# Kernel tuning notes

Measured on AMD Instinct MI355X. Metric: run time of the kernel, lower is better.

Reference implementation:

```python
import jax, jax.numpy as jnp
import numpy as np

N_IMG = 1024
N_VIEWS = 90


def _bilinear(img, yi, xi):
    """Bilinear sample img at float coords (yi=row, xi=col); 0 outside (skimage warp cval=0)."""
    n = img.shape[0]
    y0 = jnp.floor(yi)
    x0 = jnp.floor(xi)
    wy = yi - y0
    wx = xi - x0
    y0i = y0.astype(jnp.int32)
    x0i = x0.astype(jnp.int32)

    def get(yy, xx):
        valid = (yy >= 0) & (yy < n) & (xx >= 0) & (xx < n)
        v = img[jnp.clip(yy, 0, n - 1), jnp.clip(xx, 0, n - 1)]
        return jnp.where(valid, v, jnp.zeros((), img.dtype))

    v00 = get(y0i, x0i)
    v01 = get(y0i, x0i + 1)
    v10 = get(y0i + 1, x0i)
    v11 = get(y0i + 1, x0i + 1)
    return (v00 * (1 - wy) * (1 - wx) + v01 * (1 - wy) * wx
            + v10 * wy * (1 - wx) + v11 * wy * wx)


def radon_jax(image, theta_deg):
    """skimage.transform.radon(image, theta, circle=True) equivalent.
    Rotate image by each angle (bilinear, about center = N//2, inverse map as in
    skimage warp) and sum over rows. Returns sinogram [N, n_angles]."""
    n = image.shape[0]
    center = n // 2
    ang = jnp.deg2rad(theta_deg.astype(image.dtype))
    cos_a = jnp.cos(ang)  # [A]
    sin_a = jnp.sin(ang)
    coords = jnp.arange(n, dtype=image.dtype)
    X, Y = jnp.meshgrid(coords, coords)  # X = col (x), Y = row (y), [N, N]

    def rotate_and_sum(ca, sa):
        # inverse map: src = R @ dst (homogeneous, (x, y) order) as in skimage radon
        x_in = ca * X + sa * Y - center * (ca + sa - 1)
        y_in = -sa * X + ca * Y - center * (ca - sa - 1)
        rotated = _bilinear(image, y_in, x_in)  # [N, N]
        return rotated.sum(axis=0)  # sum over rows -> projection [N]

    sino = jax.vmap(rotate_and_sum)(cos_a, sin_a)  # [A, N]
    return sino.T  # [N, A] to match skimage radon layout


def setup_inputs() -> dict:
    key = jax.random.key(0)
    k1, _ = jax.random.split(key)
    x = jax.random.normal(k1, (N_IMG, N_IMG), dtype=jnp.float32)
    theta = jnp.arange(N_VIEWS, dtype=jnp.float32) * 2.0  # 0..178 deg, 2-deg spacing
    return {"x": x, "theta": theta}


def reference(x, theta):
    return radon_jax(x, theta)
```

## Files before the change

kernel.cpp:

```cpp
#include <hip/hip_runtime.h>

#define N_IMG   1024
#define N_VIEWS 90
#define CENTER  512
#define NTHREADS 512
#define NWAVES   8
#define JOBS     16
#define JOBH     32
#define YPT      (JOBH / NWAVES)
#define BUF_WORDS 5120

typedef float v2f __attribute__((ext_vector_type(2)));

__device__ __forceinline__ void map_coords(float ca, float sa, float cx, float cy,
                                           float Xf, float Yf,
                                           float& x_in, float& y_in) {
    const float fx0 = fmaf(ca, Xf, cx);
    const float fy0 = fmaf(-sa, Xf, cy);
    x_in = fmaf(sa, Yf, fx0);
    y_in = fmaf(ca, Yf, fy0);
}

__device__ __forceinline__ void gload_lds4(const float* g, float* l) {
    __builtin_amdgcn_global_load_lds((const __attribute__((address_space(1))) void*)g,
                                     (__attribute__((address_space(3))) void*)l, 4, 0, 0);
}

template<int STRIDE>
__device__ __forceinline__ float sample_tile(const float* __restrict__ tile,
                                             float sa, float ca,
                                             float x_in, float y_in, float basef) {
    const float Sf = (float)STRIDE;
    v2f x2 = {x_in, x_in + sa};
    v2f y2 = {y_in, y_in + ca};
    const v2f dx2 = {2.0f * sa, 2.0f * sa};
    const v2f dy2 = {2.0f * ca, 2.0f * ca};
    const v2f S2  = {Sf, Sf};
    const v2f b2  = {basef, basef};
    v2f acc2 = {0.0f, 0.0f};
    #pragma unroll
    for (int p = 0; p < YPT / 2; ++p) {
        v2f x0f = {floorf(x2.x), floorf(x2.y)};
        v2f y0f = {floorf(y2.x), floorf(y2.y)};
        const v2f wx = x2 - x0f;
        const v2f wy = y2 - y0f;
        const v2f lif = y0f * S2 + x0f + b2;
        const int li0 = (int)lif.x;
        const int li1 = (int)lif.y;
        const v2f t00 = {tile[li0],              tile[li1]};
        const v2f t01 = {tile[li0 + 1],          tile[li1 + 1]};
        const v2f t10 = {tile[li0 + STRIDE],     tile[li1 + STRIDE]};
        const v2f t11 = {tile[li0 + STRIDE + 1], tile[li1 + STRIDE + 1]};
        const v2f top = (t01 - t00) * wx + t00;
        const v2f bot = (t11 - t10) * wx + t10;
        acc2 += (bot - top) * wy + top;
        x2 += dx2; y2 += dy2;
    }
    return acc2.x + acc2.y;
}

__global__ __launch_bounds__(NTHREADS, 8) void radon_fused(const float* __restrict__ img,
                                                           const float* __restrict__ theta,
                                                           float* __restrict__ out) {
    __shared__ float tile[2][BUF_WORDS];

    const int tx = blockIdx.x;
    const int h  = blockIdx.y;
    const int a  = blockIdx.z;
    const int X0 = tx * 64;
    const int Y0 = h * (JOBS * JOBH);
    const int tid  = threadIdx.x;
    const int lane = tid & 63;
    const int wv   = tid >> 6;

    const float ang = theta[a] * 0.017453292519943295f;
    float sa, ca;
    __sincosf(ang, &sa, &ca);
    const float cx = (float)CENTER * (1.0f - ca - sa);
    const float cy = (float)CENTER * (1.0f - ca + sa);
    const bool pathA = (fabsf(ca) >= fabsf(sa));
    const int S = pathA ? 74 : 70;

    const int jj = lane & (JOBS - 1);
    const float Yb = (float)(Y0 + jj * JOBH);
    float x00, y00, x01, y01, x10, y10, x11, y11;
    map_coords(ca, sa, cx, cy, (float)X0,        Yb,         x00, y00);
    map_coords(ca, sa, cx, cy, (float)(X0 + 63), Yb,         x01, y01);
    map_coords(ca, sa, cx, cy, (float)X0,        Yb + 31.f,  x10, y10);
    map_coords(ca, sa, cx, cy, (float)(X0 + 63), Yb + 31.f,  x11, y11);
    const float xmin = fminf(fminf(x00, x01), fminf(x10, x11));
    const float xmax = fmaxf(fmaxf(x00, x01), fmaxf(x10, x11));
    const float ymin = fminf(fminf(y00, y01), fminf(y10, y11));
    const float ymax = fmaxf(fmaxf(y00, y01), fmaxf(y10, y11));

    const int ix0 = (int)floorf(xmin);
    const int ix1 = (int)floorf(xmax) + 1;
    const int gy0 = (int)floorf(ymin);
    const int gy1 = (int)floorf(ymax) + 1;

    const bool empty = (ix1 < 0) || (ix0 > N_IMG - 1) ||
                       (gy1 < 0) || (gy0 > N_IMG - 1);
    const bool interior = (ix0 >= 0) && (ix1 <= N_IMG - 1) &&
                          (gy0 >= 0) && (gy1 <= N_IMG - 1);

    const int winl = interior ? min(ix0, N_IMG - 64) : ix0;
    const int dBl  = max(0, ix1 - 63 - winl);
    const int nrl  = gy1 - gy0 + 1;
    const int iy0l = gy0;
    const int fll  = empty ? 1 : (interior ? 2 : 0);

    int wn, dn, yn, nn, fn;
    auto fetch = [&](int j) {
        wn = __shfl(winl, j); dn = __shfl(dBl, j);
        yn = __shfl(iy0l, j); nn = __shfl(nrl, j); fn = __shfl(fll, j);
    };

    auto stage = [&](int win, int dB, int py0, int nrows, int fl, float* buf) {
        if (fl == 1) return;
        if (fl == 2) {
            const float* g = img + (size_t)(py0 + wv) * N_IMG + win + lane;
            float* l = buf + wv * S;
            for (int r = wv; r < nrows; r += NWAVES) {
                gload_lds4(g, l);
                if (dB > 0) gload_lds4(g + dB, l + dB);
                g += NWAVES * N_IMG;
                l += NWAVES * S;
            }
        } else {
            for (int r = wv; r < nrows; r += NWAVES) {
                const int gy = py0 + r;
                const bool rOK = ((unsigned)gy < (unsigned)N_IMG);
                const int gx = win + lane;
                const float* gp = img + (size_t)gy * N_IMG;
                float* l = buf + r * S;
                if (rOK && (unsigned)gx < (unsigned)N_IMG) gload_lds4(gp + gx, l);
                else l[lane] = 0.0f;
                if (dB > 0) {
                    const int gx2 = gx + dB;
                    if (rOK && (unsigned)gx2 < (unsigned)N_IMG) gload_lds4(gp + gx2, l + dB);
                    else l[dB + lane] = 0.0f;
                }
            }
        }
    };

    const float Xf  = (float)(X0 + lane);
    const float fx0 = fmaf(ca, Xf, cx);
    const float fy0 = fmaf(-sa, Xf, cy);
    float acc = 0.0f;

    fetch(0);
    int wc = wn, dc = dn, yc = yn, nc = nn, fc = fn;
    stage(wc, dc, yc, nc, fc, tile[0]);
    __syncthreads();

    for (int j = 0; j < JOBS; ++j) {
        if (j < JOBS - 1) {
            fetch(j + 1);
            stage(wn, dn, yn, nn, fn, tile[(j + 1) & 1]);
        }
        if (fc != 1) {
            const float Ybf  = (float)(Y0 + j * JOBH + wv * YPT);
            const float x_in = fmaf(sa, Ybf, fx0);
            const float y_in = fmaf(ca, Ybf, fy0);
            const float basef = -(float)(yc * S + wc);
            const float* tl = tile[j & 1];
            acc += pathA ? sample_tile<74>(tl, sa, ca, x_in, y_in, basef)
                         : sample_tile<70>(tl, sa, ca, x_in, y_in, basef);
        }
        __syncthreads();
        wc = wn; dc = dn; yc = yn; nc = nn; fc = fn;
    }

    tile[0][wv * 64 + lane] = acc;
    __syncthreads();
    if (wv == 0) {
        float s = 0.0f;
        #pragma unroll
        for (int w = 0; w < NWAVES; ++w) s += tile[0][w * 64 + lane];
        atomicAdd(&out[(X0 + lane) * N_VIEWS + a], s);
    }
}

extern "C" void kernel_launch(void* const* d_in, const int* in_sizes, int n_in,
                              void* d_out, int out_size, void* d_ws, size_t ws_size,
                              hipStream_t stream) {
    const float* img   = (const float*)d_in[0];
    const float* theta = (const float*)d_in[1];
    float* out = (float*)d_out;
    (void)d_ws; (void)ws_size;

    (void)hipMemsetAsync(d_out, 0, (size_t)out_size * sizeof(float), stream);
    radon_fused<<<dim3(16, 2, N_VIEWS), NTHREADS, 0, stream>>>(img, theta, out);
}
```

Measured before the change: 157.1 us.

## Restructure radon into per-wave independent segments with angle-sized LDS windows

Replaces the block-cooperative double-buffered tile pipeline with independent per-wave work items. Each wave covers 32 columns by 128 rows and stages small 16-row windows into its own LDS slice using 16-byte global-to-LDS loads. The window width is chosen per angle from a few templated sizes, which cuts staged bytes and removes block-wide barriers. The cost is losing cross-wave load/compute overlap, since each wave waits on vmcnt(0) before sampling, and issuing more atomics from a larger grid.

```diff
diff --git a/kernel.cpp b/kernel.cpp
--- a/kernel.cpp
+++ b/kernel.cpp
@@ -1,14 +1,12 @@
 #include <hip/hip_runtime.h>
 
-#define N_IMG   1024
-#define N_VIEWS 90
-#define CENTER  512
-#define NTHREADS 512
-#define NWAVES   8
-#define JOBS     16
-#define JOBH     32
-#define YPT      (JOBH / NWAVES)
-#define BUF_WORDS 5120
+#define N_IMG    1024
+#define N_VIEWS  90
+#define CENTER   512
+#define NTHREADS 256
+#define NWAVES   4
+#define BUFW     1536
+#define NJOBS    8
 
 typedef float v2f __attribute__((ext_vector_type(2)));
 
@@ -25,12 +23,16 @@
     __builtin_amdgcn_global_load_lds((const __attribute__((address_space(1))) void*)g,
                                      (__attribute__((address_space(3))) void*)l, 4, 0, 0);
 }
+__device__ __forceinline__ void gload_lds16(const float* g, float* l) {
+    __builtin_amdgcn_global_load_lds((const __attribute__((address_space(1))) void*)g,
+                                     (__attribute__((address_space(3))) void*)l, 16, 0, 0);
+}
 
-template<int STRIDE>
-__device__ __forceinline__ float sample_tile(const float* __restrict__ tile,
-                                             float sa, float ca,
-                                             float x_in, float y_in, float basef) {
-    const float Sf = (float)STRIDE;
+template<int P>
+__device__ __forceinline__ float sample8(const float* __restrict__ tile,
+                                         float sa, float ca,
+                                         float x_in, float y_in, float basef) {
+    const float Sf = (float)P;
     v2f x2 = {x_in, x_in + sa};
     v2f y2 = {y_in, y_in + ca};
     const v2f dx2 = {2.0f * sa, 2.0f * sa};
@@ -39,7 +41,7 @@
     const v2f b2  = {basef, basef};
     v2f acc2 = {0.0f, 0.0f};
     #pragma unroll
-    for (int p = 0; p < YPT / 2; ++p) {
+    for (int p = 0; p < 4; ++p) {
         v2f x0f = {floorf(x2.x), floorf(x2.y)};
         v2f y0f = {floorf(y2.x), floorf(y2.y)};
         const v2f wx = x2 - x0f;
@@ -47,10 +49,10 @@
         const v2f lif = y0f * S2 + x0f + b2;
         const int li0 = (int)lif.x;
         const int li1 = (int)lif.y;
-        const v2f t00 = {tile[li0],              tile[li1]};
-        const v2f t01 = {tile[li0 + 1],          tile[li1 + 1]};
-        const v2f t10 = {tile[li0 + STRIDE],     tile[li1 + STRIDE]};
-        const v2f t11 = {tile[li0 + STRIDE + 1], tile[li1 + STRIDE + 1]};
+        const v2f t00 = {tile[li0],          tile[li1]};
+        const v2f t01 = {tile[li0 + 1],      tile[li1 + 1]};
+        const v2f t10 = {tile[li0 + P],      tile[li1 + P]};
+        const v2f t11 = {tile[li0 + P + 1],  tile[li1 + P + 1]};
         const v2f top = (t01 - t00) * wx + t00;
         const v2f bot = (t11 - t10) * wx + t10;
         acc2 += (bot - top) * wy + top;
@@ -59,127 +61,115 @@
     return acc2.x + acc2.y;
 }
 
-__global__ __launch_bounds__(NTHREADS, 8) void radon_fused(const float* __restrict__ img,
+template<int P, int WS>
+__device__ float run_seg(const float* __restrict__ img, float* __restrict__ buf,
+                         float sa, float ca, float cx, float cy,
+                         int X0i, int Ys, int lane) {
+    const float Xf  = (float)(X0i + (lane & 31));
+    const float fx0 = fmaf(ca, Xf, cx);
+    const float fy0 = fmaf(-sa, Xf, cy);
+    const int  yoff = (lane >> 5) << 3;
+    const float Xc0 = (float)X0i, Xc1 = (float)(X0i + 31);
+    float acc = 0.0f;
+
+    for (int jj = 0; jj < NJOBS; ++jj) {
+        const float Y0f = (float)(Ys + jj * 16);
+        const float Y1f = Y0f + 15.0f;
+        float x00, y00, x01, y01, x10, y10, x11, y11;
+        map_coords(ca, sa, cx, cy, Xc0, Y0f, x00, y00);
+        map_coords(ca, sa, cx, cy, Xc1, Y0f, x01, y01);
+        map_coords(ca, sa, cx, cy, Xc0, Y1f, x10, y10);
+        map_coords(ca, sa, cx, cy, Xc1, Y1f, x11, y11);
+        const float xmin = fminf(fminf(x00, x01), fminf(x10, x11));
+        const float xmax = fmaxf(fmaxf(x00, x01), fmaxf(x10, x11));
+        const float ymin = fminf(fminf(y00, y01), fminf(y10, y11));
+        const float ymax = fmaxf(fmaxf(y00, y01), fmaxf(y10, y11));
+        const int ix0 = (int)floorf(xmin);
+        const int ix1 = (int)floorf(xmax) + 1;
+        const int iy0 = (int)floorf(ymin);
+        const int iy1 = (int)floorf(ymax) + 1;
+
+        if (ix1 < 0 || ix0 > N_IMG - 1 || iy1 < 0 || iy0 > N_IMG - 1)
+            continue;
+
+        int win = ix0 & ~3;
+        const bool interior = (ix0 >= 0) && (ix1 <= N_IMG - 1) &&
+                              (iy0 >= 0) && (iy1 <= N_IMG - 1);
+        const int R = iy1 - iy0 + 1;
+
+        if (interior) {
+            win = min(win, N_IMG - WS);
+            int gb = iy0 * N_IMG + win;
+            float* lb = buf;
+            for (int r = 0; r < R; ++r) {
+                if (lane < WS / 4)
+                    gload_lds16(img + gb + 4 * lane, lb);
+                gb += N_IMG;
+                lb += P;
+            }
+        } else {
+            const int D = R * P;
+            for (int d0 = lane; d0 < D; d0 += 64) {
+                const int r  = (int)((unsigned)d0 / (unsigned)P);
+                const int c  = d0 - r * P;
+                const int gy = iy0 + r;
+                const int gx = win + c;
+                float* lb = buf + (d0 - lane);
+                if ((unsigned)gy < (unsigned)N_IMG && (unsigned)gx < (unsigned)N_IMG)
+                    gload_lds4(img + (size_t)gy * N_IMG + gx, lb);
+                else
+                    buf[d0] = 0.0f;
+            }
+        }
+        asm volatile("s_waitcnt vmcnt(0)" ::: "memory");
+
+        const float Ybf  = Y0f + (float)yoff;
+        const float x_in = fmaf(sa, Ybf, fx0);
+        const float y_in = fmaf(ca, Ybf, fy0);
+        const float basef = -(float)(iy0 * P + win);
+        acc += sample8<P>(buf, sa, ca, x_in, y_in, basef);
+    }
+    return acc;
+}
+
+__global__ __launch_bounds__(NTHREADS, 6) void radon_waves(const float* __restrict__ img,
                                                            const float* __restrict__ theta,
                                                            float* __restrict__ out) {
-    __shared__ float tile[2][BUF_WORDS];
+    __shared__ float lds[NWAVES][BUFW];
 
-    const int tx = blockIdx.x;
-    const int h  = blockIdx.y;
-    const int a  = blockIdx.z;
-    const int X0 = tx * 64;
-    const int Y0 = h * (JOBS * JOBH);
     const int tid  = threadIdx.x;
     const int lane = tid & 63;
     const int wv   = tid >> 6;
+    const int wid  = blockIdx.x * NWAVES + wv;
+    const int a    = wid >> 8;
+    const int rem  = wid & 255;
+    const int X0   = (rem & 31) << 5;
+    const int Ys   = (rem >> 5) << 7;
 
     const float ang = theta[a] * 0.017453292519943295f;
     float sa, ca;
     __sincosf(ang, &sa, &ca);
     const float cx = (float)CENTER * (1.0f - ca - sa);
     const float cy = (float)CENTER * (1.0f - ca + sa);
-    const bool pathA = (fabsf(ca) >= fabsf(sa));
-    const int S = pathA ? 74 : 70;
 
-    const int jj = lane & (JOBS - 1);
-    const float Yb = (float)(Y0 + jj * JOBH);
-    float x00, y00, x01, y01, x10, y10, x11, y11;
-    map_coords(ca, sa, cx, cy, (float)X0,        Yb,         x00, y00);
-    map_coords(ca, sa, cx, cy, (float)(X0 + 63), Yb,         x01, y01);
-    map_coords(ca, sa, cx, cy, (float)X0,        Yb + 31.f,  x10, y10);
-    map_coords(ca, sa, cx, cy, (float)(X0 + 63), Yb + 31.f,  x11, y11);
-    const float xmin = fminf(fminf(x00, x01), fminf(x10, x11));
-    const float xmax = fmaxf(fmaxf(x00, x01), fmaxf(x10, x11));
-    const float ymin = fminf(fminf(y00, y01), fminf(y10, y11));
-    const float ymax = fmaxf(fmaxf(y00, y01), fmaxf(y10, y11));
+    const float aca = fabsf(ca), asa = fabsf(sa);
+    const int Wneed = (int)ceilf(fmaf(31.0f, aca, 15.0f * asa)) + 5;
+    const int cls   = ((Wneed + 3) >> 2) - 5;
+    float* buf = &lds[wv][0];
 
-    const int ix0 = (int)floorf(xmin);
-    const int ix1 = (int)floorf(xmax) + 1;
-    const int gy0 = (int)floorf(ymin);
-    const int gy1 = (int)floorf(ymax) + 1;
-
-    const bool empty = (ix1 < 0) || (ix0 > N_IMG - 1) ||
-                       (gy1 < 0) || (gy0 > N_IMG - 1);
-    const bool interior = (ix0 >= 0) && (ix1 <= N_IMG - 1) &&
-                          (gy0 >= 0) && (gy1 <= N_IMG - 1);
-
-    const int winl = interior ? min(ix0, N_IMG - 64) : ix0;
-    const int dBl  = max(0, ix1 - 63 - winl);
-    const int nrl  = gy1 - gy0 + 1;
-    const int iy0l = gy0;
-    const int fll  = empty ? 1 : (interior ? 2 : 0);
-
-    int wn, dn, yn, nn, fn;
-    auto fetch = [&](int j) {
-        wn = __shfl(winl, j); dn = __shfl(dBl, j);
-        yn = __shfl(iy0l, j); nn = __shfl(nrl, j); fn = __shfl(fll, j);
-    };
-
-    auto stage = [&](int win, int dB, int py0, int nrows, int fl, float* buf) {
-        if (fl == 1) return;
-        if (fl == 2) {
-            const float* g = img + (size_t)(py0 + wv) * N_IMG + win + lane;
-            float* l = buf + wv * S;
-            for (int r = wv; r < nrows; r += NWAVES) {
-                gload_lds4(g, l);
-                if (dB > 0) gload_lds4(g + dB, l + dB);
-                g += NWAVES * N_IMG;
-                l += NWAVES * S;
-            }
-        } else {
-            for (int r = wv; r < nrows; r += NWAVES) {
-                const int gy = py0 + r;
-                const bool rOK = ((unsigned)gy < (unsigned)N_IMG);
-                const int gx = win + lane;
-                const float* gp = img + (size_t)gy * N_IMG;
-                float* l = buf + r * S;
-                if (rOK && (unsigned)gx < (unsigned)N_IMG) gload_lds4(gp + gx, l);
-                else l[lane] = 0.0f;
-                if (dB > 0) {
-                    const int gx2 = gx + dB;
-                    if (rOK && (unsigned)gx2 < (unsigned)N_IMG) gload_lds4(gp + gx2, l + dB);
-                    else l[dB + lane] = 0.0f;
-                }
-            }
-        }
-    };
-
-    const float Xf  = (float)(X0 + lane);
-    const float fx0 = fmaf(ca, Xf, cx);
-    const float fy0 = fmaf(-sa, Xf, cy);
-    float acc = 0.0f;
-
-    fetch(0);
-    int wc = wn, dc = dn, yc = yn, nc = nn, fc = fn;
-    stage(wc, dc, yc, nc, fc, tile[0]);
-    __syncthreads();
-
-    for (int j = 0; j < JOBS; ++j) {
-        if (j < JOBS - 1) {
-            fetch(j + 1);
-            stage(wn, dn, yn, nn, fn, tile[(j + 1) & 1]);
-        }
-        if (fc != 1) {
-            const float Ybf  = (float)(Y0 + j * JOBH + wv * YPT);
-            const float x_in = fmaf(sa, Ybf, fx0);
-            const float y_in = fmaf(ca, Ybf, fy0);
-            const float basef = -(float)(yc * S + wc);
-            const float* tl = tile[j & 1];
-            acc += pathA ? sample_tile<74>(tl, sa, ca, x_in, y_in, basef)
-                         : sample_tile<70>(tl, sa, ca, x_in, y_in, basef);
-        }
-        __syncthreads();
-        wc = wn; dc = dn; yc = yn; nc = nn; fc = fn;
+    float acc;
+    switch (cls) {
+        case 0:  acc = run_seg<21, 20>(img, buf, sa, ca, cx, cy, X0, Ys, lane); break;
+        case 1:  acc = run_seg<25, 24>(img, buf, sa, ca, cx, cy, X0, Ys, lane); break;
+        case 2:  acc = run_seg<29, 28>(img, buf, sa, ca, cx, cy, X0, Ys, lane); break;
+        case 3:  acc = run_seg<33, 32>(img, buf, sa, ca, cx, cy, X0, Ys, lane); break;
+        case 4:  acc = run_seg<37, 36>(img, buf, sa, ca, cx, cy, X0, Ys, lane); break;
+        default: acc = run_seg<41, 40>(img, buf, sa, ca, cx, cy, X0, Ys, lane); break;
     }
 
-    tile[0][wv * 64 + lane] = acc;
-    __syncthreads();
-    if (wv == 0) {
-        float s = 0.0f;
-        #pragma unroll
-        for (int w = 0; w < NWAVES; ++w) s += tile[0][w * 64 + lane];
-        atomicAdd(&out[(X0 + lane) * N_VIEWS + a], s);
-    }
+    const float tot = acc + __shfl_xor(acc, 32);
+    if (lane < 32)
+        atomicAdd(&out[(size_t)(X0 + lane) * N_VIEWS + a], tot);
 }
 
 extern "C" void kernel_launch(void* const* d_in, const int* in_sizes, int n_in,
@@ -191,5 +181,5 @@
     (void)d_ws; (void)ws_size;
 
     (void)hipMemsetAsync(d_out, 0, (size_t)out_size * sizeof(float), stream);
-    radon_fused<<<dim3(16, 2, N_VIEWS), NTHREADS, 0, stream>>>(img, theta, out);
+    radon_waves<<<dim3(23040 / NWAVES), NTHREADS, 0, stream>>>(img, theta, out);
 }
```

Result: slower. 240.2 us (+52.9%).
